# Performance work log

Hardware: AMD Instinct MI355X
Metric: run time of the kernel (lower is better)

The kernel has to match this reference:

```python
import jax, jax.numpy as jnp
import numpy as np


def setup_inputs() -> dict:
    key = jax.random.key(0)
    k1, k2 = jax.random.split(key)
    B, N, M, D = 16, 2048, 2048, 3
    predictions = jax.random.normal(k1, (B, N, D), dtype=jnp.float32)
    targets = jax.random.normal(k2, (B, M, D), dtype=jnp.float32)
    return {"predictions": predictions, "targets": targets}


def reference(predictions, targets):
    # Batched pairwise squared distances: [B, N, M]
    # d(i,j) = |x_i|^2 + |y_j|^2 - 2 x_i . y_j
    xx = jnp.sum(predictions * predictions, axis=-1)  # [B, N]
    yy = jnp.sum(targets * targets, axis=-1)          # [B, M]
    xy = jnp.einsum("bnd,bmd->bnm", predictions, targets)  # [B, N, M]
    P = xx[:, :, None] + yy[:, None, :] - 2.0 * xy    # [B, N, M]
    # Chamfer: sum of per-point nearest-neighbor squared distances, both directions
    loss = jnp.sum(jnp.min(P, axis=2)) + jnp.sum(jnp.min(P, axis=1))
    return loss
```

## Files before the change

### kernel.cpp

```cpp
#include <hip/hip_runtime.h>
#include <math.h>


#define BATCH   16
#define NPTS    2048
#define KSLICE  16
#define SLICE   128
#define SPT     8

__global__ void zero_out_kernel(float* out) { out[0] = 0.0f; }

__global__ __launch_bounds__(256) void chamfer_partial(
    const float* __restrict__ preds,
    const float* __restrict__ tgts,
    float* __restrict__ partial)
{
    __shared__ float4 q[SLICE];

    const int bid   = blockIdx.x;
    const int combo = bid & 31;
    const int slice = bid >> 5;
    const int dir   = combo >> 4;
    const int b     = combo & 15;

    const float* src = (dir ? tgts : preds) + (size_t)b * NPTS * 3;
    const float* opp = (dir ? preds : tgts) + (size_t)b * NPTS * 3;

    if (threadIdx.x < SLICE) {
        const int jj = slice * SLICE + threadIdx.x;
        const float y0 = opp[3 * jj + 0];
        const float y1 = opp[3 * jj + 1];
        const float y2 = opp[3 * jj + 2];
        q[threadIdx.x] = make_float4(y0, y1, y2, y0 * y0 + y1 * y1 + y2 * y2);
    }

    float n0[SPT], n1[SPT], n2[SPT], m[SPT];
    #pragma unroll
    for (int k = 0; k < SPT; k++) {
        const int i = threadIdx.x + 256 * k;
        n0[k] = -2.0f * src[3 * i + 0];
        n1[k] = -2.0f * src[3 * i + 1];
        n2[k] = -2.0f * src[3 * i + 2];
        m[k]  = INFINITY;
    }
    __syncthreads();

    #pragma unroll 2
    for (int j = 0; j < SLICE; j++) {
        const float4 Q = q[j];
        #pragma unroll
        for (int k = 0; k < SPT; k++) {
            const float s = fmaf(n0[k], Q.x, fmaf(n1[k], Q.y, fmaf(n2[k], Q.z, Q.w)));
            m[k] = fminf(m[k], s);
        }
    }

    float* pp = partial + ((size_t)combo * KSLICE + slice) * NPTS;
    #pragma unroll
    for (int k = 0; k < SPT; k++)
        pp[threadIdx.x + 256 * k] = m[k];
}

__global__ __launch_bounds__(256) void chamfer_reduce(
    const float* __restrict__ preds,
    const float* __restrict__ tgts,
    const float* __restrict__ partial,
    float* __restrict__ out)
{
    __shared__ float wsum[4];

    const int g     = blockIdx.x * 256 + threadIdx.x;
    const int combo = g >> 11;
    const int i     = g & (NPTS - 1);
    const int dir   = combo >> 4;
    const int b     = combo & 15;

    const float* src = (dir ? tgts : preds) + (size_t)b * NPTS * 3;
    const float x0 = src[3 * i + 0];
    const float x1 = src[3 * i + 1];
    const float x2 = src[3 * i + 2];
    const float xx = x0 * x0 + x1 * x1 + x2 * x2;

    const float* pp = partial + (size_t)combo * KSLICE * NPTS + i;
    float mn = pp[0];
    #pragma unroll
    for (int s = 1; s < KSLICE; s++)
        mn = fminf(mn, pp[(size_t)s * NPTS]);

    float val = xx + mn;

    #pragma unroll
    for (int off = 32; off > 0; off >>= 1)
        val += __shfl_down(val, off, 64);

    const int lane = threadIdx.x & 63;
    const int wid  = threadIdx.x >> 6;
    if (lane == 0) wsum[wid] = val;
    __syncthreads();
    if (threadIdx.x == 0)
        atomicAdd(out, wsum[0] + wsum[1] + wsum[2] + wsum[3]);
}

extern "C" void kernel_launch(void* const* d_in, const int* in_sizes, int n_in,
                              void* d_out, int out_size, void* d_ws, size_t ws_size,
                              hipStream_t stream) {
    const float* preds = (const float*)d_in[0];
    const float* tgts  = (const float*)d_in[1];
    float* out     = (float*)d_out;
    float* partial = (float*)d_ws;

    zero_out_kernel<<<1, 1, 0, stream>>>(out);
    chamfer_partial<<<2 * BATCH * KSLICE, 256, 0, stream>>>(preds, tgts, partial);
    chamfer_reduce<<<(2 * BATCH * NPTS) / 256, 256, 0, stream>>>(preds, tgts, partial, out);
}
```

Measured before the change: 72.83 us.

## Double slice count and replace zero-kernel plus atomics with last-block reduction

Halves the per-block slice so the first kernel launches twice as many blocks (1024), which fills the GPU's compute units better. It drops the separate zero-init launch. The second kernel now writes per-block sums and uses a counter so the last block does a deterministic final reduction and stores the result. The cost is twice as much partial-min traffic in the reduce kernel, plus a fence and atomic counter per block.

```diff
diff --git a/kernel.cpp b/kernel.cpp
--- a/kernel.cpp
+++ b/kernel.cpp
@@ -4,24 +4,27 @@
 
 #define BATCH   16
 #define NPTS    2048
-#define KSLICE  16
-#define SLICE   128
+#define KSLICE  32
+#define SLICE   64
 #define SPT     8
-
-__global__ void zero_out_kernel(float* out) { out[0] = 0.0f; }
+#define NCOMBO  32
+#define NBLK2   256
 
 __global__ __launch_bounds__(256) void chamfer_partial(
     const float* __restrict__ preds,
     const float* __restrict__ tgts,
-    float* __restrict__ partial)
+    float* __restrict__ partial,
+    int* __restrict__ counter)
 {
     __shared__ float4 q[SLICE];
 
     const int bid   = blockIdx.x;
-    const int combo = bid & 31;
+    const int combo = bid & (NCOMBO - 1);
     const int slice = bid >> 5;
     const int dir   = combo >> 4;
     const int b     = combo & 15;
+
+    if (bid == 0 && threadIdx.x == 0) *counter = 0;
 
     const float* src = (dir ? tgts : preds) + (size_t)b * NPTS * 3;
     const float* opp = (dir ? preds : tgts) + (size_t)b * NPTS * 3;
@@ -65,13 +68,16 @@
     const float* __restrict__ preds,
     const float* __restrict__ tgts,
     const float* __restrict__ partial,
+    float* __restrict__ blocksum,
+    int* __restrict__ counter,
     float* __restrict__ out)
 {
     __shared__ float wsum[4];
+    __shared__ bool  amLast;
 
-    const int g     = blockIdx.x * 256 + threadIdx.x;
-    const int combo = g >> 11;
-    const int i     = g & (NPTS - 1);
+    const int idx   = blockIdx.x * 256 + threadIdx.x;
+    const int combo = idx >> 11;
+    const int i     = idx & (NPTS - 1);
     const int dir   = combo >> 4;
     const int b     = combo & 15;
 
@@ -97,8 +103,28 @@
     const int wid  = threadIdx.x >> 6;
     if (lane == 0) wsum[wid] = val;
     __syncthreads();
-    if (threadIdx.x == 0)
-        atomicAdd(out, wsum[0] + wsum[1] + wsum[2] + wsum[3]);
+
+    if (threadIdx.x == 0) {
+        const float bsum = wsum[0] + wsum[1] + wsum[2] + wsum[3];
+        __hip_atomic_store(&blocksum[blockIdx.x], bsum,
+                           __ATOMIC_RELAXED, __HIP_MEMORY_SCOPE_AGENT);
+        __threadfence();
+        amLast = (atomicAdd(counter, 1) == NBLK2 - 1);
+    }
+    __syncthreads();
+
+    if (amLast) {
+        __threadfence();
+        float v = __hip_atomic_load(&blocksum[threadIdx.x],
+                                    __ATOMIC_RELAXED, __HIP_MEMORY_SCOPE_AGENT);
+        #pragma unroll
+        for (int off = 32; off > 0; off >>= 1)
+            v += __shfl_down(v, off, 64);
+        if (lane == 0) wsum[wid] = v;
+        __syncthreads();
+        if (threadIdx.x == 0)
+            out[0] = wsum[0] + wsum[1] + wsum[2] + wsum[3];
+    }
 }
 
 extern "C" void kernel_launch(void* const* d_in, const int* in_sizes, int n_in,
@@ -106,10 +132,11 @@
                               hipStream_t stream) {
     const float* preds = (const float*)d_in[0];
     const float* tgts  = (const float*)d_in[1];
-    float* out     = (float*)d_out;
-    float* partial = (float*)d_ws;
+    float* out      = (float*)d_out;
+    float* partial  = (float*)d_ws;
+    float* blocksum = partial + (size_t)NCOMBO * KSLICE * NPTS;
+    int*   counter  = (int*)(blocksum + NBLK2);
 
-    zero_out_kernel<<<1, 1, 0, stream>>>(out);
-    chamfer_partial<<<2 * BATCH * KSLICE, 256, 0, stream>>>(preds, tgts, partial);
-    chamfer_reduce<<<(2 * BATCH * NPTS) / 256, 256, 0, stream>>>(preds, tgts, partial, out);
+    chamfer_partial<<<NCOMBO * KSLICE, 256, 0, stream>>>(preds, tgts, partial, counter);
+    chamfer_reduce<<<NBLK2, 256, 0, stream>>>(preds, tgts, partial, blocksum, counter, out);
 }
```

Result: slower. 76.90 us (+5.6%).
